# Optimization experiments

Hardware: AMD Instinct MI355X
Metric: run time of the kernel (lower is better)

Reference implementation:

```python
import jax, jax.numpy as jnp
import numpy as np

DIM = 1024
N_HEADS = 16
HEAD_DIM = DIM // N_HEADS
LN_EPS = 1e-5


def layer_norm(x, gamma, beta):
    mu = jnp.mean(x, axis=-1, keepdims=True)
    var = jnp.var(x, axis=-1, keepdims=True)
    return (x - mu) * jax.lax.rsqrt(var + LN_EPS) * gamma + beta


def setup_inputs() -> dict:
    key = jax.random.key(0)
    ks = jax.random.split(key, 12)
    B, Nq, Nc, D = 2, 2048, 2048, DIM
    s = 1.0 / np.sqrt(D)
    return {
        "query": jax.random.normal(ks[0], (B, Nq, D), jnp.float32),
        "context": jax.random.normal(ks[1], (B, Nc, D), jnp.float32),
        "Wq": jax.random.normal(ks[2], (D, D), jnp.float32) * s,
        "bq": jnp.zeros((D,), jnp.float32),
        "Wk": jax.random.normal(ks[3], (D, D), jnp.float32) * s,
        "bk": jnp.zeros((D,), jnp.float32),
        "Wv": jax.random.normal(ks[4], (D, D), jnp.float32) * s,
        "bv": jnp.zeros((D,), jnp.float32),
        "Wo": jax.random.normal(ks[5], (D, D), jnp.float32) * s,
        "bo": jnp.zeros((D,), jnp.float32),
        "gq": jnp.ones((D,), jnp.float32),
        "betaq": jnp.zeros((D,), jnp.float32),
        "gkv": jnp.ones((D,), jnp.float32),
        "betakv": jnp.zeros((D,), jnp.float32),
    }


def reference(query, context, Wq, bq, Wk, bk, Wv, bv, Wo, bo, gq, betaq, gkv, betakv):
    B, Nq, D = query.shape
    Nc = context.shape[1]
    residual = query
    q = layer_norm(query, gq, betaq)
    c = layer_norm(context, gkv, betakv)
    # projections; (B,N,D) -> (B,H,N,hd)
    Q = (q @ Wq + bq).reshape(B, Nq, N_HEADS, HEAD_DIM).transpose(0, 2, 1, 3)
    K = (c @ Wk + bk).reshape(B, Nc, N_HEADS, HEAD_DIM).transpose(0, 2, 1, 3)
    V = (c @ Wv + bv).reshape(B, Nc, N_HEADS, HEAD_DIM).transpose(0, 2, 1, 3)
    scores = jnp.einsum("bhqd,bhkd->bhqk", Q, K) / np.sqrt(HEAD_DIM).astype(np.float32)
    attn = jax.nn.softmax(scores, axis=-1)
    out = jnp.einsum("bhqk,bhkd->bhqd", attn, V)
    out = out.transpose(0, 2, 1, 3).reshape(B, Nq, D)
    return residual + out @ Wo + bo
```

## Files before the change

### kernel.cpp

```cpp
#include <hip/hip_runtime.h>
#include <hip/hip_bf16.h>

typedef unsigned short u16;
typedef unsigned long long u64;
typedef __bf16 bf16x8 __attribute__((ext_vector_type(8)));
typedef float f32x4 __attribute__((ext_vector_type(4)));

#define DIM 1024
#define NH 16
#define HD 64
#define QSCALE 0.180336880972788f

__device__ __forceinline__ u16 f2bf(float f) {
  union { float f; unsigned u; } v; v.f = f;
  unsigned r = v.u + 0x7fffu + ((v.u >> 16) & 1u);
  return (u16)(r >> 16);
}

__device__ __forceinline__ unsigned pk2(float a, float b) {
  union { __hip_bfloat162 h; unsigned u; } cv;
  cv.h = __float22bfloat162_rn(make_float2(a, b));
  return cv.u;
}

__device__ __forceinline__ float bf2f(unsigned s) {
  union { unsigned u; float f; } v; v.u = s << 16; return v.f;
}

__device__ __forceinline__ float fexp2(float x) {
#if __has_builtin(__builtin_amdgcn_exp2f)
  return __builtin_amdgcn_exp2f(x);
#else
  return exp2f(x);
#endif
}

__device__ __forceinline__ void gld16(const u16* gp, u16* lp) {
  __builtin_amdgcn_global_load_lds(
      (const __attribute__((address_space(1))) unsigned int*)(const void*)gp,
      (__attribute__((address_space(3))) unsigned int*)(void*)lp, 16, 0, 0);
}

__global__ __launch_bounds__(256) void prep_kernel(
    const float* __restrict__ q, const float* __restrict__ c,
    const float* __restrict__ gq, const float* __restrict__ bq,
    const float* __restrict__ gkv, const float* __restrict__ bkv,
    u16* __restrict__ qn, u16* __restrict__ cn,
    const float* W0, const float* W1, const float* W2, const float* W3,
    u16* O0, u16* O1, u16* O2, u16* O3) {
  __shared__ float red[2][4];
  __shared__ float t[32][33];
  int bid = blockIdx.x, tid = threadIdx.x;
  if (bid < 8192) {
    const float* x  = bid < 4096 ? q : c;
    const float* g  = bid < 4096 ? gq : gkv;
    const float* be = bid < 4096 ? bq : bkv;
    u16* out = bid < 4096 ? qn : cn;
    int row = bid & 4095;
    float4 v = ((const float4*)(x + (size_t)row * DIM))[tid];
    float s1 = v.x + v.y + v.z + v.w;
    float s2 = v.x * v.x + v.y * v.y + v.z * v.z + v.w * v.w;
#pragma unroll
    for (int o = 32; o >= 1; o >>= 1) { s1 += __shfl_xor(s1, o, 64); s2 += __shfl_xor(s2, o, 64); }
    int wv = tid >> 6;
    if ((tid & 63) == 0) { red[0][wv] = s1; red[1][wv] = s2; }
    __syncthreads();
    s1 = red[0][0] + red[0][1] + red[0][2] + red[0][3];
    s2 = red[1][0] + red[1][1] + red[1][2] + red[1][3];
    float mu = s1 * (1.f / DIM);
    float var = s2 * (1.f / DIM) - mu * mu;
    float rs = rsqrtf(var + 1e-5f);
    float4 gv = ((const float4*)g)[tid];
    float4 bv = ((const float4*)be)[tid];
    uint2 o2;
    o2.x = pk2((v.x - mu) * rs * gv.x + bv.x, (v.y - mu) * rs * gv.y + bv.y);
    o2.y = pk2((v.z - mu) * rs * gv.z + bv.z, (v.w - mu) * rs * gv.w + bv.w);
    ((uint2*)(out + (size_t)row * DIM))[tid] = o2;
  } else {
    int wid = bid - 8192;
    int z = wid >> 10;
    const float* W = z == 0 ? W0 : z == 1 ? W1 : z == 2 ? W2 : W3;
    u16* O        = z == 0 ? O0 : z == 1 ? O1 : z == 2 ? O2 : O3;
    int xy = wid & 1023;
    int bx = (xy & 31) * 32, by = (xy >> 5) * 32;
    int tx = tid & 31, ty = tid >> 5;
#pragma unroll
    for (int i = 0; i < 4; ++i) t[ty + i * 8][tx] = W[(size_t)(by + ty + i * 8) * DIM + bx + tx];
    __syncthreads();
#pragma unroll
    for (int i = 0; i < 4; ++i) O[(size_t)(bx + ty + i * 8) * DIM + by + tx] = f2bf(t[tx][ty + i * 8]);
  }
}

__global__ __launch_bounds__(256) void gemm_qkv(
    const u16* __restrict__ qn, const u16* __restrict__ cn,
    const u16* __restrict__ Wqt, const u16* __restrict__ Wkt, const u16* __restrict__ Wvt,
    const float* __restrict__ bq, const float* __restrict__ bk, const float* __restrict__ bv,
    u16* __restrict__ Qb, u16* __restrict__ Kb, u16* __restrict__ Vtb) {
  __shared__ __align__(16) u16 sm[(128 + 64 + 64) * 64];
  u16* As  = sm;
  u16* B0s = sm + 128 * 64;
  u16* B1s = sm + 192 * 64;
  int tid = threadIdx.x, wave = tid >> 6, lane = tid & 63;
  int lr = lane & 15, quad = lane >> 4;
  int m0 = blockIdx.x * 128, n0 = blockIdx.y * 64;
  int wm = (wave >> 1) * 64, wn = (wave & 1) * 32;

  if (blockIdx.z == 0) {
    f32x4 acck[4][2] = {}, accv[4][2] = {};
    for (int kt = 0; kt < DIM; kt += 64) {
#pragma unroll
      for (int r = 0; r < 4; ++r) {
        int slot = tid + r * 256;
        int row = slot >> 3;
        int c = (slot & 7) ^ (row & 7);
        gld16(cn + (size_t)(m0 + row) * DIM + kt + c * 8, &As[slot * 8]);
      }
      {
        int slot = tid;
        int row = slot >> 3;
        int c = (slot & 7) ^ (row & 7);
        gld16(Wkt + (size_t)(n0 + row) * DIM + kt + c * 8, &B0s[slot * 8]);
        gld16(Wvt + (size_t)(n0 + row) * DIM + kt + c * 8, &B1s[slot * 8]);
        slot = tid + 256; row = slot >> 3; c = (slot & 7) ^ (row & 7);
        gld16(Wkt + (size_t)(n0 + row) * DIM + kt + c * 8, &B0s[slot * 8]);
        gld16(Wvt + (size_t)(n0 + row) * DIM + kt + c * 8, &B1s[slot * 8]);
      }
      __syncthreads();
#pragma unroll
      for (int kc = 0; kc < 2; ++kc) {
        int pc = ((kc * 4 + quad) ^ (lr & 7)) * 8;
        bf16x8 af[4], b0f[2], b1f[2];
#pragma unroll
        for (int i = 0; i < 4; ++i) af[i] = *(const bf16x8*)&As[(wm + i * 16 + lr) * 64 + pc];
#pragma unroll
        for (int j = 0; j < 2; ++j) {
          b0f[j] = *(const bf16x8*)&B0s[(wn + j * 16 + lr) * 64 + pc];
          b1f[j] = *(const bf16x8*)&B1s[(wn + j * 16 + lr) * 64 + pc];
        }
#pragma unroll
        for (int mi = 0; mi < 4; ++mi)
#pragma unroll
          for (int ni = 0; ni < 2; ++ni) {
            acck[mi][ni] = __builtin_amdgcn_mfma_f32_16x16x32_bf16(af[mi], b0f[ni], acck[mi][ni], 0, 0, 0);
            accv[mi][ni] = __builtin_amdgcn_mfma_f32_16x16x32_bf16(b1f[ni], af[mi], accv[mi][ni], 0, 0, 0);
          }
      }
      __syncthreads();
    }
#pragma unroll
    for (int mi = 0; mi < 4; ++mi)
#pragma unroll
      for (int ni = 0; ni < 2; ++ni) {
        int col = n0 + wn + ni * 16 + lr;
        float bb_ = bk[col];
        int row0 = m0 + wm + mi * 16 + quad * 4;
#pragma unroll
        for (int r = 0; r < 4; ++r)
          Kb[(size_t)(row0 + r) * DIM + col] = f2bf(acck[mi][ni][r] + bb_);
      }
#pragma unroll
    for (int mi = 0; mi < 4; ++mi) {
      int m = m0 + wm + mi * 16 + lr;
      int bb = m >> 11, tt = m & 2047;
      u16* outb = Vtb + (((size_t)bb << 10)) * 2048 + tt;
#pragma unroll
      for (int ni = 0; ni < 2; ++ni) {
        int nbase = n0 + wn + ni * 16 + quad * 4;
#pragma unroll
        for (int r = 0; r < 4; ++r)
          outb[(size_t)(nbase + r) * 2048] = f2bf(accv[mi][ni][r] + bv[nbase + r]);
      }
    }
  } else {
    f32x4 acc[4][2] = {};
    for (int kt = 0; kt < DIM; kt += 64) {
#pragma unroll
      for (int r = 0; r < 4; ++r) {
        int slot = tid + r * 256;
        int row = slot >> 3;
        int c = (slot & 7) ^ (row & 7);
        gld16(qn + (size_t)(m0 + row) * DIM + kt + c * 8, &As[slot * 8]);
      }
#pragma unroll
      for (int r = 0; r < 2; ++r) {
        int slot = tid + r * 256;
        int row = slot >> 3;
        int c = (slot & 7) ^ (row & 7);
        gld16(Wqt + (size_t)(n0 + row) * DIM + kt + c * 8, &B0s[slot * 8]);
      }
      __syncthreads();
#pragma unroll
      for (int kc = 0; kc < 2; ++kc) {
        int pc = ((kc * 4 + quad) ^ (lr & 7)) * 8;
        bf16x8 af[4], b0f[2];
#pragma unroll
        for (int i = 0; i < 4; ++i) af[i] = *(const bf16x8*)&As[(wm + i * 16 + lr) * 64 + pc];
#pragma unroll
        for (int j = 0; j < 2; ++j) b0f[j] = *(const bf16x8*)&B0s[(wn + j * 16 + lr) * 64 + pc];
#pragma unroll
        for (int mi = 0; mi < 4; ++mi)
#pragma unroll
          for (int ni = 0; ni < 2; ++ni)
            acc[mi][ni] = __builtin_amdgcn_mfma_f32_16x16x32_bf16(af[mi], b0f[ni], acc[mi][ni], 0, 0, 0);
      }
      __syncthreads();
    }
#pragma unroll
    for (int mi = 0; mi < 4; ++mi)
#pragma unroll
      for (int ni = 0; ni < 2; ++ni) {
        int col = n0 + wn + ni * 16 + lr;
        float bb_ = bq[col];
        int row0 = m0 + wm + mi * 16 + quad * 4;
#pragma unroll
        for (int r = 0; r < 4; ++r)
          Qb[(size_t)(row0 + r) * DIM + col] = f2bf((acc[mi][ni][r] + bb_) * QSCALE);
      }
  }
}

__global__ __launch_bounds__(256) void gemm_o(const u16* __restrict__ A,
    const u16* __restrict__ Bt, const float* __restrict__ bias,
    float* __restrict__ out, const float* __restrict__ resid) {
  __shared__ __align__(16) u16 sm[(128 + 64) * 64];
  u16* As = sm;
  u16* Bs = sm + 128 * 64;
  int tid = threadIdx.x, wave = tid >> 6, lane = tid & 63;
  int lr = lane & 15, quad = lane >> 4;
  int m0 = blockIdx.x * 128, n0 = blockIdx.y * 64;
  int wm = (wave >> 1) * 64, wn = (wave & 1) * 32;
  f32x4 acc[4][2] = {};
  for (int kt = 0; kt < DIM; kt += 64) {
#pragma unroll
    for (int r = 0; r < 4; ++r) {
      int slot = tid + r * 256;
      int row = slot >> 3;
      int c = (slot & 7) ^ (row & 7);
      gld16(A + (size_t)(m0 + row) * DIM + kt + c * 8, &As[slot * 8]);
    }
#pragma unroll
    for (int r = 0; r < 2; ++r) {
      int slot = tid + r * 256;
      int row = slot >> 3;
      int c = (slot & 7) ^ (row & 7);
      gld16(Bt + (size_t)(n0 + row) * DIM + kt + c * 8, &Bs[slot * 8]);
    }
    __syncthreads();
#pragma unroll
    for (int kc = 0; kc < 2; ++kc) {
      int pc = ((kc * 4 + quad) ^ (lr & 7)) * 8;
      bf16x8 af[4], bfr[2];
#pragma unroll
      for (int i = 0; i < 4; ++i) af[i] = *(const bf16x8*)&As[(wm + i * 16 + lr) * 64 + pc];
#pragma unroll
      for (int j = 0; j < 2; ++j) bfr[j] = *(const bf16x8*)&Bs[(wn + j * 16 + lr) * 64 + pc];
#pragma unroll
      for (int mi = 0; mi < 4; ++mi)
#pragma unroll
        for (int ni = 0; ni < 2; ++ni)
          acc[mi][ni] = __builtin_amdgcn_mfma_f32_16x16x32_bf16(af[mi], bfr[ni], acc[mi][ni], 0, 0, 0);
    }
    __syncthreads();
  }
#pragma unroll
  for (int mi = 0; mi < 4; ++mi)
#pragma unroll
    for (int ni = 0; ni < 2; ++ni) {
      int col = n0 + wn + ni * 16 + lr;
      float bv = bias[col];
      int row0 = m0 + wm + mi * 16 + quad * 4;
#pragma unroll
      for (int r = 0; r < 4; ++r) {
        int row = row0 + r;
        out[(size_t)row * DIM + col] = acc[mi][ni][r] + bv + resid[(size_t)row * DIM + col];
      }
    }
}

__global__ __launch_bounds__(256) void flash_kernel(const u16* __restrict__ Q,
    const u16* __restrict__ Kg, const u16* __restrict__ Vt,
    u16* __restrict__ O0, u16* __restrict__ O1,
    float* __restrict__ L0, float* __restrict__ L1) {
  __shared__ __align__(16) u16 lds[24576];
  int tid = threadIdx.x, wave = tid >> 6, lane = tid & 63;
  int lr = lane & 15, quad = lane >> 4;
  int bh = blockIdx.x, b = bh >> 4, h = bh & 15;
  int q0 = blockIdx.y * 128;
  int split = blockIdx.z;
  u16* Op = split ? O1 : O0;
  float* Lp = split ? L1 : L0;
  int t0 = split * 1024;

  const u16* kbase = Kg + (size_t)(b * 2048 + t0) * DIM + h * HD;
  const u16* vbase = Vt + (size_t)(b * 1024 + h * HD) * 2048 + t0;

  bf16x8 qf[2][2];
#pragma unroll
  for (int s = 0; s < 2; ++s)
#pragma unroll
    for (int kc = 0; kc < 2; ++kc)
      qf[s][kc] = *(const bf16x8*)&Q[((size_t)(b * 2048 + q0 + wave * 32 + s * 16 + lr)) * DIM +
                                     h * HD + kc * 32 + quad * 8];

  int slot0 = tid, slot1 = tid + 256;
  int r0 = slot0 >> 3, c0 = (slot0 & 7) ^ (r0 & 7);
  int r1 = slot1 >> 3, c1 = (slot1 & 7) ^ (r1 & 7);
  const u16* kp0 = kbase + (size_t)r0 * DIM + c0 * 8;
  const u16* kp1 = kbase + (size_t)r1 * DIM + c1 * 8;
  const u16* vp0 = vbase + (size_t)r0 * 2048 + c0 * 8;
  const u16* vp1 = vbase + (size_t)r1 * 2048 + c1 * 8;

  gld16(kp0, &lds[slot0 * 8]);
  gld16(kp1, &lds[slot1 * 8]);
  gld16(vp0, &lds[8192 + slot0 * 8]);
  gld16(vp1, &lds[8192 + slot1 * 8]);
  __syncthreads();

  u16* Pw = &lds[16384 + wave * 2048];
  float plsum[2] = {0.f, 0.f};
  f32x4 oacc[2][4] = {};

  for (int j = 0; j < 16; ++j) {
    int par = j & 1;
    const u16* kcb = &lds[par * 4096];
    const u16* vcb = &lds[8192 + par * 4096];
    if (j < 15) {
      int np = par ^ 1;
      kp0 += 64 * DIM; kp1 += 64 * DIM; vp0 += 64; vp1 += 64;
      gld16(kp0, &lds[np * 4096 + slot0 * 8]);
      gld16(kp1, &lds[np * 4096 + slot1 * 8]);
      gld16(vp0, &lds[8192 + np * 4096 + slot0 * 8]);
      gld16(vp1, &lds[8192 + np * 4096 + slot1 * 8]);
    }

    f32x4 sf[2][4] = {};
#pragma unroll
    for (int kc = 0; kc < 2; ++kc) {
      int pc = ((kc * 4 + quad) ^ (lr & 7)) * 8;
#pragma unroll
      for (int ns = 0; ns < 4; ++ns) {
        bf16x8 kf = *(const bf16x8*)&kcb[(ns * 16 + lr) * 64 + pc];
#pragma unroll
        for (int s = 0; s < 2; ++s)
          sf[s][ns] = __builtin_amdgcn_mfma_f32_16x16x32_bf16(kf, qf[s][kc], sf[s][ns], 0, 0, 0);
      }
    }

#pragma unroll
    for (int s = 0; s < 2; ++s)
#pragma unroll
      for (int ns = 0; ns < 4; ++ns) {
        float p0 = fexp2(sf[s][ns][0]), p1 = fexp2(sf[s][ns][1]);
        float p2 = fexp2(sf[s][ns][2]), p3 = fexp2(sf[s][ns][3]);
        plsum[s] += (p0 + p1) + (p2 + p3);
        uint2 pk;
        pk.x = pk2(p0, p1);
        pk.y = pk2(p2, p3);
        int chunk = ns * 2 + (quad >> 1);
        int off = (s * 16 + lr) * 64 + ((chunk ^ (lr & 7)) * 8) + (quad & 1) * 4;
        *(uint2*)&Pw[off] = pk;
      }
    __threadfence_block();

#pragma unroll
    for (int kc = 0; kc < 2; ++kc) {
      int pc = ((kc * 4 + quad) ^ (lr & 7)) * 8;
      bf16x8 pf[2];
#pragma unroll
      for (int s = 0; s < 2; ++s)
        pf[s] = *(const bf16x8*)&Pw[(s * 16 + lr) * 64 + pc];
#pragma unroll
      for (int ds = 0; ds < 4; ++ds) {
        bf16x8 vf = *(const bf16x8*)&vcb[(ds * 16 + lr) * 64 + pc];
#pragma unroll
        for (int s = 0; s < 2; ++s)
          oacc[s][ds] = __builtin_amdgcn_mfma_f32_16x16x32_bf16(vf, pf[s], oacc[s][ds], 0, 0, 0);
      }
    }
    __syncthreads();
  }

#pragma unroll
  for (int s = 0; s < 2; ++s) {
    float l = plsum[s];
    l += __shfl_xor(l, 16, 64);
    l += __shfl_xor(l, 32, 64);
    size_t qrow = (size_t)(b * 2048 + q0 + wave * 32 + s * 16 + lr);
    if (quad == 0) Lp[qrow * 16 + h] = l;
#pragma unroll
    for (int ds = 0; ds < 4; ++ds) {
      uint2 pk;
      pk.x = pk2(oacc[s][ds][0], oacc[s][ds][1]);
      pk.y = pk2(oacc[s][ds][2], oacc[s][ds][3]);
      *(uint2*)&Op[qrow * DIM + h * HD + ds * 16 + quad * 4] = pk;
    }
  }
}

__global__ __launch_bounds__(256) void combine_kernel(const u16* __restrict__ O0,
    const u16* __restrict__ O1, const float* __restrict__ L0, const float* __restrict__ L1,
    u16* __restrict__ AO) {
  int row = blockIdx.x, tid = threadIdx.x;
  int h = tid >> 4;
  float rl = 1.f / (L0[row * 16 + h] + L1[row * 16 + h]);
  uint2 a = ((const uint2*)(O0 + (size_t)row * DIM))[tid];
  uint2 b = ((const uint2*)(O1 + (size_t)row * DIM))[tid];
  float v0 = (bf2f(a.x & 0xffff) + bf2f(b.x & 0xffff)) * rl;
  float v1 = (bf2f(a.x >> 16)    + bf2f(b.x >> 16))    * rl;
  float v2 = (bf2f(a.y & 0xffff) + bf2f(b.y & 0xffff)) * rl;
  float v3 = (bf2f(a.y >> 16)    + bf2f(b.y >> 16))    * rl;
  uint2 o;
  o.x = pk2(v0, v1);
  o.y = pk2(v2, v3);
  ((uint2*)(AO + (size_t)row * DIM))[tid] = o;
}

extern "C" void kernel_launch(void* const* d_in, const int* in_sizes, int n_in,
                              void* d_out, int out_size, void* d_ws, size_t ws_size,
                              hipStream_t stream) {
  const float* query   = (const float*)d_in[0];
  const float* context = (const float*)d_in[1];
  const float* Wq = (const float*)d_in[2];
  const float* bq = (const float*)d_in[3];
  const float* Wk = (const float*)d_in[4];
  const float* bk = (const float*)d_in[5];
  const float* Wv = (const float*)d_in[6];
  const float* bv = (const float*)d_in[7];
  const float* Wo = (const float*)d_in[8];
  const float* bo = (const float*)d_in[9];
  const float* gq    = (const float*)d_in[10];
  const float* betaq = (const float*)d_in[11];
  const float* gkv   = (const float*)d_in[12];
  const float* betakv= (const float*)d_in[13];
  (void)in_sizes; (void)n_in; (void)out_size; (void)ws_size;

  char* ws = (char*)d_ws;
  const size_t MB = (size_t)1 << 20;
  u16* qn  = (u16*)(ws + 0 * MB);
  u16* cn  = (u16*)(ws + 8 * MB);
  u16* Wqt = (u16*)(ws + 16 * MB);
  u16* Wkt = (u16*)(ws + 18 * MB);
  u16* Wvt = (u16*)(ws + 20 * MB);
  u16* Wot = (u16*)(ws + 22 * MB);
  u16* Qb  = (u16*)(ws + 24 * MB);
  u16* Kb  = (u16*)(ws + 32 * MB);
  u16* Vtb = (u16*)(ws + 40 * MB);
  u16* AOb = (u16*)(ws + 48 * MB);
  u16* Op0 = qn;
  u16* Op1 = cn;
  float* L0 = (float*)(ws + 16 * MB);
  float* L1 = (float*)(ws + 16 * MB + 256 * 1024);

  prep_kernel<<<12288, 256, 0, stream>>>(query, context, gq, betaq, gkv, betakv,
                                         qn, cn, Wq, Wk, Wv, Wo, Wqt, Wkt, Wvt, Wot);

  gemm_qkv<<<dim3(32, 16, 2), 256, 0, stream>>>(qn, cn, Wqt, Wkt, Wvt,
                                                bq, bk, bv, Qb, Kb, Vtb);

  flash_kernel<<<dim3(32, 16, 2), 256, 0, stream>>>(Qb, Kb, Vtb, Op0, Op1, L0, L1);

  combine_kernel<<<4096, 256, 0, stream>>>(Op0, Op1, L0, L1, AOb);

  gemm_o<<<dim3(32, 16), 256, 0, stream>>>(AOb, Wot, bo, (float*)d_out, query);
}
```

Before: 220.9 us.

## Double-buffer A tiles in LDS and prefetch B fragments directly into registers

The projection GEMMs now double-buffer the A tile in LDS, issuing the next k-step's async global-to-LDS loads before computing on the current buffer. The weight (B) fragments skip LDS entirely: each lane loads its MFMA operand straight from global memory into registers, prefetched one iteration ahead. This overlaps memory latency with MFMA work and removes the B staging, at the cost of more registers and uncoalesced-ish per-lane 16-byte B loads. The loop is fully unrolled over 16 k-steps.

```diff
diff --git a/kernel.cpp b/kernel.cpp
--- a/kernel.cpp
+++ b/kernel.cpp
@@ -40,6 +40,8 @@
       (const __attribute__((address_space(1))) unsigned int*)(const void*)gp,
       (__attribute__((address_space(3))) unsigned int*)(void*)lp, 16, 0, 0);
 }
+
+__device__ __forceinline__ bf16x8 ld8(const u16* p) { return *(const bf16x8*)p; }
 
 __global__ __launch_bounds__(256) void prep_kernel(
     const float* __restrict__ q, const float* __restrict__ c,
@@ -97,56 +99,80 @@
     const u16* __restrict__ Wqt, const u16* __restrict__ Wkt, const u16* __restrict__ Wvt,
     const float* __restrict__ bq, const float* __restrict__ bk, const float* __restrict__ bv,
     u16* __restrict__ Qb, u16* __restrict__ Kb, u16* __restrict__ Vtb) {
-  __shared__ __align__(16) u16 sm[(128 + 64 + 64) * 64];
-  u16* As  = sm;
-  u16* B0s = sm + 128 * 64;
-  u16* B1s = sm + 192 * 64;
+  __shared__ __align__(16) u16 As[2][128 * 64];
   int tid = threadIdx.x, wave = tid >> 6, lane = tid & 63;
   int lr = lane & 15, quad = lane >> 4;
   int m0 = blockIdx.x * 128, n0 = blockIdx.y * 64;
   int wm = (wave >> 1) * 64, wn = (wave & 1) * 32;
 
+  const u16* Ain = blockIdx.z ? qn : cn;
+  const u16* ap[4];
+  int sl[4];
+#pragma unroll
+  for (int r = 0; r < 4; ++r) {
+    int slot = tid + r * 256;
+    int row = slot >> 3;
+    int c = (slot & 7) ^ (row & 7);
+    sl[r] = slot * 8;
+    ap[r] = Ain + (size_t)(m0 + row) * DIM + c * 8;
+  }
+
   if (blockIdx.z == 0) {
+    const u16* bp0[2][2];
+    const u16* bp1[2][2];
+#pragma unroll
+    for (int ni = 0; ni < 2; ++ni)
+#pragma unroll
+      for (int kc = 0; kc < 2; ++kc) {
+        size_t off = (size_t)(n0 + wn + ni * 16 + lr) * DIM + kc * 32 + quad * 8;
+        bp0[ni][kc] = Wkt + off;
+        bp1[ni][kc] = Wvt + off;
+      }
     f32x4 acck[4][2] = {}, accv[4][2] = {};
-    for (int kt = 0; kt < DIM; kt += 64) {
-#pragma unroll
-      for (int r = 0; r < 4; ++r) {
-        int slot = tid + r * 256;
-        int row = slot >> 3;
-        int c = (slot & 7) ^ (row & 7);
-        gld16(cn + (size_t)(m0 + row) * DIM + kt + c * 8, &As[slot * 8]);
-      }
-      {
-        int slot = tid;
-        int row = slot >> 3;
-        int c = (slot & 7) ^ (row & 7);
-        gld16(Wkt + (size_t)(n0 + row) * DIM + kt + c * 8, &B0s[slot * 8]);
-        gld16(Wvt + (size_t)(n0 + row) * DIM + kt + c * 8, &B1s[slot * 8]);
-        slot = tid + 256; row = slot >> 3; c = (slot & 7) ^ (row & 7);
-        gld16(Wkt + (size_t)(n0 + row) * DIM + kt + c * 8, &B0s[slot * 8]);
-        gld16(Wvt + (size_t)(n0 + row) * DIM + kt + c * 8, &B1s[slot * 8]);
-      }
-      __syncthreads();
+#pragma unroll
+    for (int r = 0; r < 4; ++r) gld16(ap[r], &As[0][sl[r]]);
+    bf16x8 b0c[2][2], b1c[2][2];
+#pragma unroll
+    for (int ni = 0; ni < 2; ++ni)
+#pragma unroll
+      for (int kc = 0; kc < 2; ++kc) { b0c[ni][kc] = ld8(bp0[ni][kc]); b1c[ni][kc] = ld8(bp1[ni][kc]); }
+    __syncthreads();
+#pragma unroll
+    for (int j = 0; j < 16; ++j) {
+      int par = j & 1;
+      bf16x8 b0n[2][2], b1n[2][2];
+      if (j < 15) {
+#pragma unroll
+        for (int r = 0; r < 4; ++r) gld16(ap[r] + (j + 1) * 64, &As[par ^ 1][sl[r]]);
+#pragma unroll
+        for (int ni = 0; ni < 2; ++ni)
+#pragma unroll
+          for (int kc = 0; kc < 2; ++kc) {
+            b0n[ni][kc] = ld8(bp0[ni][kc] + (j + 1) * 64);
+            b1n[ni][kc] = ld8(bp1[ni][kc] + (j + 1) * 64);
+          }
+      }
 #pragma unroll
       for (int kc = 0; kc < 2; ++kc) {
         int pc = ((kc * 4 + quad) ^ (lr & 7)) * 8;
-        bf16x8 af[4], b0f[2], b1f[2];
-#pragma unroll
-        for (int i = 0; i < 4; ++i) af[i] = *(const bf16x8*)&As[(wm + i * 16 + lr) * 64 + pc];
-#pragma unroll
-        for (int j = 0; j < 2; ++j) {
-          b0f[j] = *(const bf16x8*)&B0s[(wn + j * 16 + lr) * 64 + pc];
-          b1f[j] = *(const bf16x8*)&B1s[(wn + j * 16 + lr) * 64 + pc];
-        }
+        bf16x8 af[4];
+#pragma unroll
+        for (int i = 0; i < 4; ++i) af[i] = *(const bf16x8*)&As[par][(wm + i * 16 + lr) * 64 + pc];
 #pragma unroll
         for (int mi = 0; mi < 4; ++mi)
 #pragma unroll
           for (int ni = 0; ni < 2; ++ni) {
-            acck[mi][ni] = __builtin_amdgcn_mfma_f32_16x16x32_bf16(af[mi], b0f[ni], acck[mi][ni], 0, 0, 0);
-            accv[mi][ni] = __builtin_amdgcn_mfma_f32_16x16x32_bf16(b1f[ni], af[mi], accv[mi][ni], 0, 0, 0);
+            acck[mi][ni] = __builtin_amdgcn_mfma_f32_16x16x32_bf16(af[mi], b0c[ni][kc], acck[mi][ni], 0, 0, 0);
+            accv[mi][ni] = __builtin_amdgcn_mfma_f32_16x16x32_bf16(b1c[ni][kc], af[mi], accv[mi][ni], 0, 0, 0);
           }
       }
       __syncthreads();
+      if (j < 15) {
+#pragma unroll
+        for (int ni = 0; ni < 2; ++ni)
+#pragma unroll
+          for (int kc = 0; kc < 2; ++kc) { b0c[ni][kc] = b0n[ni][kc]; b1c[ni][kc] = b1n[ni][kc]; }
+      }
     }
 #pragma unroll
     for (int mi = 0; mi < 4; ++mi)
@@ -173,38 +199,52 @@
       }
     }
   } else {
+    const u16* bp[2][2];
+#pragma unroll
+    for (int ni = 0; ni < 2; ++ni)
+#pragma unroll
+      for (int kc = 0; kc < 2; ++kc)
+        bp[ni][kc] = Wqt + (size_t)(n0 + wn + ni * 16 + lr) * DIM + kc * 32 + quad * 8;
     f32x4 acc[4][2] = {};
-    for (int kt = 0; kt < DIM; kt += 64) {
-#pragma unroll
-      for (int r = 0; r < 4; ++r) {
-        int slot = tid + r * 256;
-        int row = slot >> 3;
-        int c = (slot & 7) ^ (row & 7);
-        gld16(qn + (size_t)(m0 + row) * DIM + kt + c * 8, &As[slot * 8]);
-      }
-#pragma unroll
-      for (int r = 0; r < 2; ++r) {
-        int slot = tid + r * 256;
-        int row = slot >> 3;
-        int c = (slot & 7) ^ (row & 7);
-        gld16(Wqt + (size_t)(n0 + row) * DIM + kt + c * 8, &B0s[slot * 8]);
-      }
-      __syncthreads();
+#pragma unroll
+    for (int r = 0; r < 4; ++r) gld16(ap[r], &As[0][sl[r]]);
+    bf16x8 bc[2][2];
+#pragma unroll
+    for (int ni = 0; ni < 2; ++ni)
+#pragma unroll
+      for (int kc = 0; kc < 2; ++kc) bc[ni][kc] = ld8(bp[ni][kc]);
+    __syncthreads();
+#pragma unroll
+    for (int j = 0; j < 16; ++j) {
+      int par = j & 1;
+      bf16x8 bn[2][2];
+      if (j < 15) {
+#pragma unroll
+        for (int r = 0; r < 4; ++r) gld16(ap[r] + (j + 1) * 64, &As[par ^ 1][sl[r]]);
+#pragma unroll
+        for (int ni = 0; ni < 2; ++ni)
+#pragma unroll
+          for (int kc = 0; kc < 2; ++kc) bn[ni][kc] = ld8(bp[ni][kc] + (j + 1) * 64);
+      }
 #pragma unroll
       for (int kc = 0; kc < 2; ++kc) {
         int pc = ((kc * 4 + quad) ^ (lr & 7)) * 8;
-        bf16x8 af[4], b0f[2];
-#pragma unroll
-        for (int i = 0; i < 4; ++i) af[i] = *(const bf16x8*)&As[(wm + i * 16 + lr) * 64 + pc];
-#pragma unroll
-        for (int j = 0; j < 2; ++j) b0f[j] = *(const bf16x8*)&B0s[(wn + j * 16 + lr) * 64 + pc];
+        bf16x8 af[4];
+#pragma unroll
+        for (int i = 0; i < 4; ++i) af[i] = *(const bf16x8*)&As[par][(wm + i * 16 + lr) * 64 + pc];
 #pragma unroll
         for (int mi = 0; mi < 4; ++mi)
 #pragma unroll
           for (int ni = 0; ni < 2; ++ni)
-            acc[mi][ni] = __builtin_amdgcn_mfma_f32_16x16x32_bf16(af[mi], b0f[ni], acc[mi][ni], 0, 0, 0);
+            acc[mi][ni] = __builtin_amdgcn_mfma_f32_16x16x32_bf16(af[mi], bc[ni][kc], acc[mi][ni], 0, 0, 0);
       }
       __syncthreads();
+      if (j < 15) {
+#pragma unroll
+        for (int ni = 0; ni < 2; ++ni)
+#pragma unroll
+          for (int kc = 0; kc < 2; ++kc) bc[ni][kc] = bn[ni][kc];
+      }
     }
 #pragma unroll
     for (int mi = 0; mi < 4; ++mi)
@@ -223,45 +263,67 @@
 __global__ __launch_bounds__(256) void gemm_o(const u16* __restrict__ A,
     const u16* __restrict__ Bt, const float* __restrict__ bias,
     float* __restrict__ out, const float* __restrict__ resid) {
-  __shared__ __align__(16) u16 sm[(128 + 64) * 64];
-  u16* As = sm;
-  u16* Bs = sm + 128 * 64;
+  __shared__ __align__(16) u16 As[2][128 * 64];
   int tid = threadIdx.x, wave = tid >> 6, lane = tid & 63;
   int lr = lane & 15, quad = lane >> 4;
   int m0 = blockIdx.x * 128, n0 = blockIdx.y * 64;
   int wm = (wave >> 1) * 64, wn = (wave & 1) * 32;
+  const u16* ap[4];
+  int sl[4];
+#pragma unroll
+  for (int r = 0; r < 4; ++r) {
+    int slot = tid + r * 256;
+    int row = slot >> 3;
+    int c = (slot & 7) ^ (row & 7);
+    sl[r] = slot * 8;
+    ap[r] = A + (size_t)(m0 + row) * DIM + c * 8;
+  }
+  const u16* bp[2][2];
+#pragma unroll
+  for (int ni = 0; ni < 2; ++ni)
+#pragma unroll
+    for (int kc = 0; kc < 2; ++kc)
+      bp[ni][kc] = Bt + (size_t)(n0 + wn + ni * 16 + lr) * DIM + kc * 32 + quad * 8;
   f32x4 acc[4][2] = {};
-  for (int kt = 0; kt < DIM; kt += 64) {
-#pragma unroll
-    for (int r = 0; r < 4; ++r) {
-      int slot = tid + r * 256;
-      int row = slot >> 3;
-      int c = (slot & 7) ^ (row & 7);
-      gld16(A + (size_t)(m0 + row) * DIM + kt + c * 8, &As[slot * 8]);
-    }
-#pragma unroll
-    for (int r = 0; r < 2; ++r) {
-      int slot = tid + r * 256;
-      int row = slot >> 3;
-      int c = (slot & 7) ^ (row & 7);
-      gld16(Bt + (size_t)(n0 + row) * DIM + kt + c * 8, &Bs[slot * 8]);
-    }
-    __syncthreads();
+#pragma unroll
+  for (int r = 0; r < 4; ++r) gld16(ap[r], &As[0][sl[r]]);
+  bf16x8 bc[2][2];
+#pragma unroll
+  for (int ni = 0; ni < 2; ++ni)
+#pragma unroll
+    for (int kc = 0; kc < 2; ++kc) bc[ni][kc] = ld8(bp[ni][kc]);
+  __syncthreads();
+#pragma unroll
+  for (int j = 0; j < 16; ++j) {
+    int par = j & 1;
+    bf16x8 bn[2][2];
+    if (j < 15) {
+#pragma unroll
+      for (int r = 0; r < 4; ++r) gld16(ap[r] + (j + 1) * 64, &As[par ^ 1][sl[r]]);
+#pragma unroll
+      for (int ni = 0; ni < 2; ++ni)
+#pragma unroll
+        for (int kc = 0; kc < 2; ++kc) bn[ni][kc] = ld8(bp[ni][kc] + (j + 1) * 64);
+    }
 #pragma unroll
     for (int kc = 0; kc < 2; ++kc) {
       int pc = ((kc * 4 + quad) ^ (lr & 7)) * 8;
-      bf16x8 af[4], bfr[2];
-#pragma unroll
-      for (int i = 0; i < 4; ++i) af[i] = *(const bf16x8*)&As[(wm + i * 16 + lr) * 64 + pc];
-#pragma unroll
-      for (int j = 0; j < 2; ++j) bfr[j] = *(const bf16x8*)&Bs[(wn + j * 16 + lr) * 64 + pc];
+      bf16x8 af[4];
+#pragma unroll
+      for (int i = 0; i < 4; ++i) af[i] = *(const bf16x8*)&As[par][(wm + i * 16 + lr) * 64 + pc];
 #pragma unroll
       for (int mi = 0; mi < 4; ++mi)
 #pragma unroll
         for (int ni = 0; ni < 2; ++ni)
-          acc[mi][ni] = __builtin_amdgcn_mfma_f32_16x16x32_bf16(af[mi], bfr[ni], acc[mi][ni], 0, 0, 0);
+          acc[mi][ni] = __builtin_amdgcn_mfma_f32_16x16x32_bf16(af[mi], bc[ni][kc], acc[mi][ni], 0, 0, 0);
     }
     __syncthreads();
+    if (j < 15) {
+#pragma unroll
+      for (int ni = 0; ni < 2; ++ni)
+#pragma unroll
+        for (int kc = 0; kc < 2; ++kc) bc[ni][kc] = bn[ni][kc];
+    }
   }
 #pragma unroll
   for (int mi = 0; mi < 4; ++mi)
```

Result: slower. 256.3 us (+16.0%).

## Load K fragments directly to registers and remap flash block order

Applied to the files above, without the earlier changes.

The flash kernel now loads K tiles from global memory straight into register fragments, double-buffered across two register sets, so K no longer goes through LDS. Only V stays in LDS, which cuts shared memory per block from 48KB to 32KB and can raise occupancy. The loop is unrolled by two with a macro so the register buffers can alternate. The grid is also flattened and remapped so that consecutive block IDs spread across batch-head pairs, likely to improve L2 locality or XCD distribution. The cost is more VGPR pressure and uncoalesced 16-byte global K loads per lane.

```diff
diff --git a/kernel.cpp b/kernel.cpp
--- a/kernel.cpp
+++ b/kernel.cpp
@@ -40,6 +40,8 @@
       (const __attribute__((address_space(1))) unsigned int*)(const void*)gp,
       (__attribute__((address_space(3))) unsigned int*)(void*)lp, 16, 0, 0);
 }
+
+__device__ __forceinline__ bf16x8 ld8(const u16* p) { return *(const bf16x8*)p; }
 
 __global__ __launch_bounds__(256) void prep_kernel(
     const float* __restrict__ q, const float* __restrict__ c,
@@ -282,17 +284,19 @@
     const u16* __restrict__ Kg, const u16* __restrict__ Vt,
     u16* __restrict__ O0, u16* __restrict__ O1,
     float* __restrict__ L0, float* __restrict__ L1) {
-  __shared__ __align__(16) u16 lds[24576];
+  __shared__ __align__(16) u16 lds[16384];
   int tid = threadIdx.x, wave = tid >> 6, lane = tid & 63;
   int lr = lane & 15, quad = lane >> 4;
-  int bh = blockIdx.x, b = bh >> 4, h = bh & 15;
-  int q0 = blockIdx.y * 128;
-  int split = blockIdx.z;
+  int bid = blockIdx.x;
+  int loc = bid >> 3;
+  int bh = ((bid & 7) << 2) | (loc >> 4);
+  int q0 = (loc & 15) * 128;
+  int b = bh >> 4, h = bh & 15;
+  int split = blockIdx.y;
   u16* Op = split ? O1 : O0;
   float* Lp = split ? L1 : L0;
   int t0 = split * 1024;
 
-  const u16* kbase = Kg + (size_t)(b * 2048 + t0) * DIM + h * HD;
   const u16* vbase = Vt + (size_t)(b * 1024 + h * HD) * 2048 + t0;
 
   bf16x8 qf[2][2];
@@ -300,86 +304,92 @@
   for (int s = 0; s < 2; ++s)
 #pragma unroll
     for (int kc = 0; kc < 2; ++kc)
-      qf[s][kc] = *(const bf16x8*)&Q[((size_t)(b * 2048 + q0 + wave * 32 + s * 16 + lr)) * DIM +
-                                     h * HD + kc * 32 + quad * 8];
+      qf[s][kc] = ld8(&Q[((size_t)(b * 2048 + q0 + wave * 32 + s * 16 + lr)) * DIM +
+                         h * HD + kc * 32 + quad * 8]);
+
+  const u16* kfb = Kg + (size_t)(b * 2048 + t0 + lr) * DIM + h * HD + quad * 8;
+  bf16x8 kA[2][4], kB[2][4];
+#pragma unroll
+  for (int kc = 0; kc < 2; ++kc)
+#pragma unroll
+    for (int ns = 0; ns < 4; ++ns)
+      kA[kc][ns] = ld8(kfb + (size_t)(ns * 16) * DIM + kc * 32);
 
   int slot0 = tid, slot1 = tid + 256;
   int r0 = slot0 >> 3, c0 = (slot0 & 7) ^ (r0 & 7);
   int r1 = slot1 >> 3, c1 = (slot1 & 7) ^ (r1 & 7);
-  const u16* kp0 = kbase + (size_t)r0 * DIM + c0 * 8;
-  const u16* kp1 = kbase + (size_t)r1 * DIM + c1 * 8;
   const u16* vp0 = vbase + (size_t)r0 * 2048 + c0 * 8;
   const u16* vp1 = vbase + (size_t)r1 * 2048 + c1 * 8;
-
-  gld16(kp0, &lds[slot0 * 8]);
-  gld16(kp1, &lds[slot1 * 8]);
-  gld16(vp0, &lds[8192 + slot0 * 8]);
-  gld16(vp1, &lds[8192 + slot1 * 8]);
+  gld16(vp0, &lds[slot0 * 8]);
+  gld16(vp1, &lds[slot1 * 8]);
   __syncthreads();
 
-  u16* Pw = &lds[16384 + wave * 2048];
+  u16* Pw = &lds[8192 + wave * 2048];
   float plsum[2] = {0.f, 0.f};
   f32x4 oacc[2][4] = {};
 
-  for (int j = 0; j < 16; ++j) {
-    int par = j & 1;
-    const u16* kcb = &lds[par * 4096];
-    const u16* vcb = &lds[8192 + par * 4096];
-    if (j < 15) {
-      int np = par ^ 1;
-      kp0 += 64 * DIM; kp1 += 64 * DIM; vp0 += 64; vp1 += 64;
-      gld16(kp0, &lds[np * 4096 + slot0 * 8]);
-      gld16(kp1, &lds[np * 4096 + slot1 * 8]);
-      gld16(vp0, &lds[8192 + np * 4096 + slot0 * 8]);
-      gld16(vp1, &lds[8192 + np * 4096 + slot1 * 8]);
-    }
-
-    f32x4 sf[2][4] = {};
-#pragma unroll
-    for (int kc = 0; kc < 2; ++kc) {
-      int pc = ((kc * 4 + quad) ^ (lr & 7)) * 8;
-#pragma unroll
-      for (int ns = 0; ns < 4; ++ns) {
-        bf16x8 kf = *(const bf16x8*)&kcb[(ns * 16 + lr) * 64 + pc];
-#pragma unroll
-        for (int s = 0; s < 2; ++s)
-          sf[s][ns] = __builtin_amdgcn_mfma_f32_16x16x32_bf16(kf, qf[s][kc], sf[s][ns], 0, 0, 0);
-      }
-    }
-
-#pragma unroll
-    for (int s = 0; s < 2; ++s)
-#pragma unroll
-      for (int ns = 0; ns < 4; ++ns) {
-        float p0 = fexp2(sf[s][ns][0]), p1 = fexp2(sf[s][ns][1]);
-        float p2 = fexp2(sf[s][ns][2]), p3 = fexp2(sf[s][ns][3]);
-        plsum[s] += (p0 + p1) + (p2 + p3);
-        uint2 pk;
-        pk.x = pk2(p0, p1);
-        pk.y = pk2(p2, p3);
-        int chunk = ns * 2 + (quad >> 1);
-        int off = (s * 16 + lr) * 64 + ((chunk ^ (lr & 7)) * 8) + (quad & 1) * 4;
-        *(uint2*)&Pw[off] = pk;
-      }
-    __threadfence_block();
-
-#pragma unroll
-    for (int kc = 0; kc < 2; ++kc) {
-      int pc = ((kc * 4 + quad) ^ (lr & 7)) * 8;
-      bf16x8 pf[2];
-#pragma unroll
-      for (int s = 0; s < 2; ++s)
-        pf[s] = *(const bf16x8*)&Pw[(s * 16 + lr) * 64 + pc];
-#pragma unroll
-      for (int ds = 0; ds < 4; ++ds) {
-        bf16x8 vf = *(const bf16x8*)&vcb[(ds * 16 + lr) * 64 + pc];
-#pragma unroll
-        for (int s = 0; s < 2; ++s)
-          oacc[s][ds] = __builtin_amdgcn_mfma_f32_16x16x32_bf16(vf, pf[s], oacc[s][ds], 0, 0, 0);
-      }
-    }
-    __syncthreads();
-  }
+#define FLASH_TILE(KCUR, KOTH, VOFF, VOTH, JNEXT, DO_PREF)                                 \
+  {                                                                                        \
+    if (DO_PREF) {                                                                         \
+      const u16* kn = kfb + (size_t)(JNEXT) * 64 * DIM;                                    \
+      _Pragma("unroll")                                                                    \
+      for (int kc = 0; kc < 2; ++kc)                                                       \
+        _Pragma("unroll")                                                                  \
+        for (int ns = 0; ns < 4; ++ns)                                                     \
+          KOTH[kc][ns] = ld8(kn + (size_t)(ns * 16) * DIM + kc * 32);                      \
+      vp0 += 64; vp1 += 64;                                                                \
+      gld16(vp0, &lds[(VOTH) + slot0 * 8]);                                                \
+      gld16(vp1, &lds[(VOTH) + slot1 * 8]);                                                \
+    }                                                                                      \
+    f32x4 sf[2][4] = {};                                                                   \
+    _Pragma("unroll")                                                                      \
+    for (int kc = 0; kc < 2; ++kc)                                                         \
+      _Pragma("unroll")                                                                    \
+      for (int ns = 0; ns < 4; ++ns)                                                       \
+        _Pragma("unroll")                                                                  \
+        for (int s = 0; s < 2; ++s)                                                        \
+          sf[s][ns] = __builtin_amdgcn_mfma_f32_16x16x32_bf16(KCUR[kc][ns], qf[s][kc],     \
+                                                              sf[s][ns], 0, 0, 0);        \
+    _Pragma("unroll")                                                                      \
+    for (int s = 0; s < 2; ++s)                                                            \
+      _Pragma("unroll")                                                                    \
+      for (int ns = 0; ns < 4; ++ns) {                                                     \
+        float p0 = fexp2(sf[s][ns][0]), p1 = fexp2(sf[s][ns][1]);                          \
+        float p2 = fexp2(sf[s][ns][2]), p3 = fexp2(sf[s][ns][3]);                          \
+        plsum[s] += (p0 + p1) + (p2 + p3);                                                 \
+        uint2 pk;                                                                          \
+        pk.x = pk2(p0, p1);                                                                \
+        pk.y = pk2(p2, p3);                                                                \
+        int chunk = ns * 2 + (quad >> 1);                                                  \
+        int off = (s * 16 + lr) * 64 + ((chunk ^ (lr & 7)) * 8) + (quad & 1) * 4;          \
+        *(uint2*)&Pw[off] = pk;                                                            \
+      }                                                                                    \
+    __threadfence_block();                                                                 \
+    _Pragma("unroll")                                                                      \
+    for (int kc = 0; kc < 2; ++kc) {                                                       \
+      int pc = ((kc * 4 + quad) ^ (lr & 7)) * 8;                                           \
+      bf16x8 pf[2];                                                                        \
+      _Pragma("unroll")                                                                    \
+      for (int s = 0; s < 2; ++s)                                                          \
+        pf[s] = *(const bf16x8*)&Pw[(s * 16 + lr) * 64 + pc];                              \
+      _Pragma("unroll")                                                                    \
+      for (int ds = 0; ds < 4; ++ds) {                                                     \
+        bf16x8 vf = *(const bf16x8*)&lds[(VOFF) + (ds * 16 + lr) * 64 + pc];               \
+        _Pragma("unroll")                                                                  \
+        for (int s = 0; s < 2; ++s)                                                        \
+          oacc[s][ds] = __builtin_amdgcn_mfma_f32_16x16x32_bf16(vf, pf[s],                 \
+                                                                oacc[s][ds], 0, 0, 0);    \
+      }                                                                                    \
+    }                                                                                      \
+    __syncthreads();                                                                       \
+  }
+
+  for (int jj = 0; jj < 8; ++jj) {
+    int j = jj * 2;
+    FLASH_TILE(kA, kB, 0, 4096, j + 1, 1);
+    FLASH_TILE(kB, kA, 4096, 0, j + 2, (jj < 7));
+  }
+#undef FLASH_TILE
 
 #pragma unroll
   for (int s = 0; s < 2; ++s) {
@@ -458,7 +468,7 @@
   gemm_qkv<<<dim3(32, 16, 2), 256, 0, stream>>>(qn, cn, Wqt, Wkt, Wvt,
                                                 bq, bk, bv, Qb, Kb, Vtb);
 
-  flash_kernel<<<dim3(32, 16, 2), 256, 0, stream>>>(Qb, Kb, Vtb, Op0, Op1, L0, L1);
+  flash_kernel<<<dim3(512, 2), 256, 0, stream>>>(Qb, Kb, Vtb, Op0, Op1, L0, L1);
 
   combine_kernel<<<4096, 256, 0, stream>>>(Op0, Op1, L0, L1, AOb);
 
```

New measurement: 244.1 us. +10.5%, slower.
